# Kernel tuning notes

Hardware: AMD Instinct MI355X
Metric: run time of the kernel (lower is better)

## Reference

```python
import jax, jax.numpy as jnp
import numpy as np

N = 50000        # nodes
DEG = 5          # avg directed degree before symmetrization
F_IN = 512       # node features
HID = 64         # hardcoded hidden width in H2GCN
C = 32           # num_classes
E1_MAX = 800000  # padded 1-hop edge count
E2_MAX = 6000000 # padded 2-hop edge count


def _pad(a, L, dtype):
    out = np.zeros(L, dtype=dtype)
    n = min(len(a), L)
    out[:n] = a[:n]
    return out


def _build_graph(seed=0):
    """Build symmetric 1-hop adjacency A1 (no self loops) and strict 2-hop A2,
    both symmetrically normalized D^-1/2 A D^-1/2, as padded COO edge lists."""
    rng = np.random.default_rng(seed)
    src = rng.integers(0, N, N * DEG)
    dst = rng.integers(0, N, N * DEG)
    row = np.concatenate([src, dst])  # symmetrize
    col = np.concatenate([dst, src])
    m = row != col                    # drop self loops (A - I > 0)
    row, col = row[m], col[m]
    key = np.unique(row.astype(np.int64) * N + col)  # dedupe, sorted by row
    row = (key // N).astype(np.int64)
    col = (key % N).astype(np.int64)
    deg = np.bincount(row, minlength=N)  # symmetric -> row sums == col sums
    dinv = np.where(deg > 0, deg.astype(np.float64) ** -0.5, 0.0).astype(np.float32)
    val1 = dinv[row] * dinv[col]
    # --- compose A@A via CSR expansion (edges sorted by row) ---
    rowptr = np.concatenate([[0], np.cumsum(deg)])
    lens = deg[col]                     # out-degree of each edge's endpoint
    total = int(lens.sum())
    starts = rowptr[col]
    grp = np.repeat(np.cumsum(lens) - lens, lens)
    idx = np.repeat(starts, lens) + (np.arange(total) - grp)
    u2 = np.repeat(row, lens)
    w2 = col[idx]
    key2 = np.unique(u2.astype(np.int64) * N + w2)
    r2 = key2 // N
    c2 = key2 % N
    # strict 2-hop: remove self loops and 1-hop edges
    keep = (r2 != c2) & (~np.isin(key2, key, assume_unique=True))
    r2, c2 = r2[keep], c2[keep]
    deg2 = np.bincount(r2, minlength=N)
    d2inv = np.where(deg2 > 0, deg2.astype(np.float64) ** -0.5, 0.0).astype(np.float32)
    val2 = d2inv[r2] * d2inv[c2]
    return (
        _pad(row, E1_MAX, np.int32), _pad(col, E1_MAX, np.int32), _pad(val1, E1_MAX, np.float32),
        _pad(r2, E2_MAX, np.int32), _pad(c2, E2_MAX, np.int32), _pad(val2, E2_MAX, np.float32),
    )


def setup_inputs() -> dict:
    key = jax.random.key(0)
    k = jax.random.split(key, 6)
    e1r, e1c, e1v, e2r, e2c, e2v = _build_graph(0)
    return {
        "x": jax.random.normal(k[0], (N, F_IN), dtype=jnp.float32),
        "e1_row": jnp.asarray(e1r), "e1_col": jnp.asarray(e1c), "e1_val": jnp.asarray(e1v),
        "e2_row": jnp.asarray(e2r), "e2_col": jnp.asarray(e2c), "e2_val": jnp.asarray(e2v),
        "W1": jax.random.normal(k[1], (F_IN, HID), dtype=jnp.float32) * (1.0 / np.sqrt(F_IN)),
        "b1": jax.random.normal(k[2], (HID,), dtype=jnp.float32) * 0.01,
        "W2": jax.random.normal(k[3], (3 * HID, C), dtype=jnp.float32) * (1.0 / np.sqrt(3 * HID)),
        "b2": jax.random.normal(k[4], (C,), dtype=jnp.float32) * 0.01,
    }


def _spmm(row, col, val, R):
    # sparse [N,N] @ dense [N,H]: gather source rows, scale, scatter-add to dest
    return jax.ops.segment_sum(val[:, None] * R[col], row, num_segments=N)


def reference(x, e1_row, e1_col, e1_val, e2_row, e2_col, e2_val, W1, b1, W2, b2):
    R = jax.nn.relu(x @ W1 + b1)            # [N, 64]
    Rs = [R]
    for _ in range(2):                       # two rounds of hop aggregation
        R1 = _spmm(e1_row, e1_col, e1_val, R)
        R2 = _spmm(e2_row, e2_col, e2_val, R)
        R = jnp.maximum(R1, R2)              # max-pool combine
        Rs.append(R)
    R_final = jnp.concatenate(Rs, axis=1)    # [N, 192]
    # dropout is identity in eval mode
    return jax.nn.log_softmax(R_final @ W2 + b2, axis=1)
```

## Files before the change

### kernel.cpp

```cpp
#include <hip/hip_runtime.h>

#define NN 50000
#define FIN 512
#define HID 64
#define NC 32

__device__ __forceinline__ unsigned short bf16rne(float f) {
  unsigned u = __float_as_uint(f);
  u = u + 0x7FFFu + ((u >> 16) & 1u);
  return (unsigned short)(u >> 16);
}
__device__ __forceinline__ float bf2f(unsigned short s) {
  return __uint_as_float(((unsigned)s) << 16);
}

__global__ __launch_bounds__(256) void gemm1_relu_kernel(
    const float* __restrict__ x, const float* __restrict__ W1,
    const float* __restrict__ b1, float* __restrict__ R0,
    unsigned short* __restrict__ R0b) {
  __shared__ float xs[32][132];
  __shared__ float wsm[32][64];
  const int t = threadIdx.x;
  const int row0 = blockIdx.x * 128;
  const int tr = t >> 4, tc = t & 15;
  float acc[8][4] = {};
  for (int k0 = 0; k0 < FIN; k0 += 32) {
#pragma unroll
    for (int j = 0; j < 4; ++j) {
      const int idx = t + j * 256;
      const int r = idx & 127, kq = idx >> 7;
      float4 xv = make_float4(0.f, 0.f, 0.f, 0.f);
      const int grow = row0 + r;
      if (grow < NN) xv = *(const float4*)(x + (size_t)grow * FIN + k0 + kq * 4);
      xs[kq * 4 + 0][r] = xv.x; xs[kq * 4 + 1][r] = xv.y;
      xs[kq * 4 + 2][r] = xv.z; xs[kq * 4 + 3][r] = xv.w;
    }
#pragma unroll
    for (int j = 0; j < 2; ++j) {
      const int idx = t + j * 256;
      const int wr = idx >> 4, wc = (idx & 15) * 4;
      *(float4*)(&wsm[wr][wc]) = *(const float4*)(W1 + (size_t)(k0 + wr) * HID + wc);
    }
    __syncthreads();
#pragma unroll
    for (int kk = 0; kk < 32; ++kk) {
      const float4 a0 = *(const float4*)(&xs[kk][tr * 8]);
      const float4 a1 = *(const float4*)(&xs[kk][tr * 8 + 4]);
      const float4 b  = *(const float4*)(&wsm[kk][tc * 4]);
      const float av[8] = {a0.x, a0.y, a0.z, a0.w, a1.x, a1.y, a1.z, a1.w};
      const float bv[4] = {b.x, b.y, b.z, b.w};
#pragma unroll
      for (int i = 0; i < 8; ++i)
#pragma unroll
        for (int j = 0; j < 4; ++j) acc[i][j] = fmaf(av[i], bv[j], acc[i][j]);
    }
    __syncthreads();
  }
  const float4 bb = *(const float4*)(b1 + tc * 4);
#pragma unroll
  for (int i = 0; i < 8; ++i) {
    const int grow = row0 + tr * 8 + i;
    if (grow < NN) {
      float4 o;
      o.x = fmaxf(acc[i][0] + bb.x, 0.f);
      o.y = fmaxf(acc[i][1] + bb.y, 0.f);
      o.z = fmaxf(acc[i][2] + bb.z, 0.f);
      o.w = fmaxf(acc[i][3] + bb.w, 0.f);
      *(float4*)(R0 + (size_t)grow * HID + tc * 4) = o;
      uint2 p;
      p.x = ((unsigned)bf16rne(o.y) << 16) | (unsigned)bf16rne(o.x);
      p.y = ((unsigned)bf16rne(o.w) << 16) | (unsigned)bf16rne(o.z);
      *(uint2*)(R0b + (size_t)grow * HID + tc * 4) = p;
    }
  }
}

__global__ void build_rowptr_kernel(const int* __restrict__ row,
                                    const float* __restrict__ val,
                                    const int E, int* __restrict__ ptr) {
  const int e = blockIdx.x * blockDim.x + threadIdx.x;
  if (e >= E) return;
  const int c = (val[e] != 0.f) ? row[e] : NN;
  const int p = (e == 0) ? -1 : ((val[e - 1] != 0.f) ? row[e - 1] : NN);
  for (int r = p + 1; r <= c; ++r) ptr[r] = e;
  if (e == E - 1) {
    for (int r = c + 1; r <= NN; ++r) ptr[r] = E;
  }
}

template <int BLK>
__device__ __forceinline__ float2 seg_pair(const int* __restrict__ col,
                                           const float* __restrict__ val,
                                           int s, int t,
                                           const unsigned short* __restrict__ Rb,
                                           uint2* __restrict__ meta,
                                           const int lane, const unsigned laneoff) {
  float a0 = 0.f, a1 = 0.f;
  const int half = lane >> 5;
  for (int e = s; e < t; e += BLK) {
    const int idx = e + lane;
    if (lane < BLK) {
      unsigned cw = 0u, vw = 0u;
      if (idx < t) { cw = (unsigned)col[idx]; vw = __float_as_uint(val[idx]); }
      meta[lane] = make_uint2(cw, vw);
    }
#pragma unroll
    for (int i = 0; i < BLK / 2; ++i) {
      const uint2 m = meta[2 * i + half];
      const float v = __uint_as_float(m.y);
      const unsigned gw =
          *(const unsigned*)((const char*)Rb + ((size_t)m.x * 128u) + laneoff);
      a0 = fmaf(v, __uint_as_float(gw << 16), a0);
      a1 = fmaf(v, __uint_as_float(gw & 0xffff0000u), a1);
    }
  }
  return make_float2(a0, a1);
}

template <int OUTMODE>
__global__ __launch_bounds__(256) void agg_kernel(
    const int* __restrict__ c1, const float* __restrict__ v1, const int* __restrict__ p1,
    const int* __restrict__ c2, const float* __restrict__ v2, const int* __restrict__ p2,
    const unsigned short* __restrict__ Rb,
    float* __restrict__ outf, unsigned short* __restrict__ outb) {
  __shared__ uint2 meta[4][64];
  const int wslot = threadIdx.x >> 6;
  const int wid = (int)((blockIdx.x * blockDim.x + threadIdx.x) >> 6);
  if (wid >= NN) return;
  const int lane = threadIdx.x & 63;
  const unsigned laneoff = (unsigned)(lane & 31) << 2;
  const float2 h1 = seg_pair<16>(c1, v1, p1[wid], p1[wid + 1], Rb, meta[wslot], lane, laneoff);
  const float2 h2 = seg_pair<64>(c2, v2, p2[wid], p2[wid + 1], Rb, meta[wslot], lane, laneoff);
  const float t1e = h1.x + __shfl_xor(h1.x, 32, 64);
  const float t1o = h1.y + __shfl_xor(h1.y, 32, 64);
  const float t2e = h2.x + __shfl_xor(h2.x, 32, 64);
  const float t2o = h2.y + __shfl_xor(h2.y, 32, 64);
  const int half = lane >> 5;
  const float r = half ? fmaxf(t1o, t2o) : fmaxf(t1e, t2e);
  const size_t oidx = (size_t)wid * HID + 2 * (lane & 31) + half;
  if (OUTMODE == 0) outb[oidx] = bf16rne(r);
  else              outf[oidx] = r;
}

__global__ void final_kernel(const float* __restrict__ R0,
                             const unsigned short* __restrict__ R1b,
                             const float* __restrict__ R2,
                             const float* __restrict__ W2,
                             const float* __restrict__ b2, float* __restrict__ out) {
  __shared__ float w2s[192 * 32];
  __shared__ float fs[8][192];
  const int t = threadIdx.x;
  const int node0 = blockIdx.x * 8;
  for (int i = t; i < 192 * 32; i += 256) w2s[i] = W2[i];
  for (int i = t; i < 8 * 192; i += 256) {
    const int n = i / 192, k = i % 192;
    const int node = node0 + n;
    float v = 0.f;
    if (node < NN) {
      v = (k < 64)  ? R0[(size_t)node * 64 + k]
        : (k < 128) ? bf2f(R1b[(size_t)node * 64 + (k - 64)])
                    : R2[(size_t)node * 64 + (k - 128)];
    }
    fs[n][k] = v;
  }
  __syncthreads();
  const int n = t >> 5, c = t & 31;
  const int node = node0 + n;
  float acc = b2[c];
#pragma unroll 8
  for (int k = 0; k < 192; ++k) acc += fs[n][k] * w2s[k * 32 + c];
  float m = acc;
  for (int off = 16; off; off >>= 1) m = fmaxf(m, __shfl_xor(m, off, 32));
  const float ex = __expf(acc - m);
  float ssum = ex;
  for (int off = 16; off; off >>= 1) ssum += __shfl_xor(ssum, off, 32);
  if (node < NN) out[(size_t)node * 32 + c] = (acc - m) - __logf(ssum);
}

extern "C" void kernel_launch(void* const* d_in, const int* in_sizes, int n_in,
                              void* d_out, int out_size, void* d_ws, size_t ws_size,
                              hipStream_t stream) {
  const float* x  = (const float*)d_in[0];
  const int*   e1r = (const int*)d_in[1];
  const int*   e1c = (const int*)d_in[2];
  const float* e1v = (const float*)d_in[3];
  const int*   e2r = (const int*)d_in[4];
  const int*   e2c = (const int*)d_in[5];
  const float* e2v = (const float*)d_in[6];
  const float* W1 = (const float*)d_in[7];
  const float* b1 = (const float*)d_in[8];
  const float* W2 = (const float*)d_in[9];
  const float* b2 = (const float*)d_in[10];
  float* out = (float*)d_out;
  const int E1 = in_sizes[1];
  const int E2 = in_sizes[4];

  char* wsb = (char*)d_ws;
  const size_t RSZ = (size_t)NN * HID;
  const size_t need = RSZ * 4 * 2 + RSZ * 2 * 2 + 2 * (NN + 1) * sizeof(int);
  if (ws_size < need) return;
  float*          R0  = (float*)wsb;
  float*          R2  = (float*)(wsb + RSZ * 4);
  unsigned short* R0b = (unsigned short*)(wsb + RSZ * 8);
  unsigned short* R1b = (unsigned short*)(wsb + RSZ * 8 + RSZ * 2);
  int*            p1  = (int*)(wsb + RSZ * 8 + RSZ * 4);
  int*            p2  = p1 + (NN + 1);

  gemm1_relu_kernel<<<(NN + 127) / 128, 256, 0, stream>>>(x, W1, b1, R0, R0b);

  build_rowptr_kernel<<<(E1 + 255) / 256, 256, 0, stream>>>(e1r, e1v, E1, p1);
  build_rowptr_kernel<<<(E2 + 255) / 256, 256, 0, stream>>>(e2r, e2v, E2, p2);

  const int aggb = (NN * 64) / 256;
  agg_kernel<0><<<aggb, 256, 0, stream>>>(e1c, e1v, p1, e2c, e2v, p2, R0b, R0, R1b);
  agg_kernel<1><<<aggb, 256, 0, stream>>>(e1c, e1v, p1, e2c, e2v, p2, R1b, R2, R1b);

  final_kernel<<<(NN + 7) / 8, 256, 0, stream>>>(R0, R1b, R2, W2, b2, out);
}
```

Measured before the change: 431.5 us.

## Use bf16 MFMA for the input projection GEMM with prepacked W1

Replaces the fp32 LDS-tiled FMA GEMM for x@W1 with a wave-level MFMA 16x16x32 bf16 kernel. x is converted to bf16 in registers, and W1 is prepacked into the MFMA B-fragment layout by a small new kernel. This aims to cut the compute and shared-memory cost of the first layer so it approaches the bandwidth of reading x. In exchange, inputs are rounded to bf16, and the prepacked buffer sits at an offset that is only 8-byte aligned.

```diff
diff --git a/kernel.cpp b/kernel.cpp
--- a/kernel.cpp
+++ b/kernel.cpp
@@ -5,6 +5,9 @@
 #define HID 64
 #define NC 32
 
+typedef __attribute__((ext_vector_type(8))) short short8;
+typedef __attribute__((ext_vector_type(4))) float f32x4;
+
 __device__ __forceinline__ unsigned short bf16rne(float f) {
   unsigned u = __float_as_uint(f);
   u = u + 0x7FFFu + ((u >> 16) & 1u);
@@ -13,66 +16,76 @@
 __device__ __forceinline__ float bf2f(unsigned short s) {
   return __uint_as_float(((unsigned)s) << 16);
 }
+__device__ __forceinline__ unsigned cvt_pk_bf16(float lo, float hi) {
+  unsigned d;
+  asm("v_cvt_pk_bf16_f32 %0, %1, %2" : "=v"(d) : "v"(lo), "v"(hi));
+  return d;
+}
+
+__global__ void w1_pack_kernel(const float* __restrict__ W1,
+                               unsigned short* __restrict__ W1p) {
+  const int t = blockIdx.x * blockDim.x + threadIdx.x;
+  if (t >= 16 * 4 * 64) return;
+  const int lane = t & 63, nb = (t >> 6) & 3, ks = t >> 8;
+  const int col = nb * 16 + (lane & 15);
+  const int k0 = ks * 32 + (lane >> 4) * 8;
+  float f[8];
+#pragma unroll
+  for (int j = 0; j < 8; ++j) f[j] = W1[(size_t)(k0 + j) * HID + col];
+  uint4 d;
+  d.x = cvt_pk_bf16(f[0], f[1]);
+  d.y = cvt_pk_bf16(f[2], f[3]);
+  d.z = cvt_pk_bf16(f[4], f[5]);
+  d.w = cvt_pk_bf16(f[6], f[7]);
+  *(uint4*)(W1p + (size_t)t * 8) = d;
+}
 
 __global__ __launch_bounds__(256) void gemm1_relu_kernel(
-    const float* __restrict__ x, const float* __restrict__ W1,
+    const float* __restrict__ x, const unsigned short* __restrict__ W1p,
     const float* __restrict__ b1, float* __restrict__ R0,
     unsigned short* __restrict__ R0b) {
-  __shared__ float xs[32][132];
-  __shared__ float wsm[32][64];
   const int t = threadIdx.x;
-  const int row0 = blockIdx.x * 128;
-  const int tr = t >> 4, tc = t & 15;
-  float acc[8][4] = {};
-  for (int k0 = 0; k0 < FIN; k0 += 32) {
+  const int w = t >> 6, lane = t & 63;
+  const int arow = blockIdx.x * 64 + w * 16 + (lane & 15);
+  const size_t rowoff = (arow < NN) ? (size_t)arow * FIN : 0;
+  const float* xp = x + rowoff + (lane >> 4) * 8;
+  f32x4 acc0 = {0.f, 0.f, 0.f, 0.f}, acc1 = acc0, acc2 = acc0, acc3 = acc0;
 #pragma unroll
-    for (int j = 0; j < 4; ++j) {
-      const int idx = t + j * 256;
-      const int r = idx & 127, kq = idx >> 7;
-      float4 xv = make_float4(0.f, 0.f, 0.f, 0.f);
-      const int grow = row0 + r;
-      if (grow < NN) xv = *(const float4*)(x + (size_t)grow * FIN + k0 + kq * 4);
-      xs[kq * 4 + 0][r] = xv.x; xs[kq * 4 + 1][r] = xv.y;
-      xs[kq * 4 + 2][r] = xv.z; xs[kq * 4 + 3][r] = xv.w;
-    }
-#pragma unroll
-    for (int j = 0; j < 2; ++j) {
-      const int idx = t + j * 256;
-      const int wr = idx >> 4, wc = (idx & 15) * 4;
-      *(float4*)(&wsm[wr][wc]) = *(const float4*)(W1 + (size_t)(k0 + wr) * HID + wc);
-    }
-    __syncthreads();
-#pragma unroll
-    for (int kk = 0; kk < 32; ++kk) {
-      const float4 a0 = *(const float4*)(&xs[kk][tr * 8]);
-      const float4 a1 = *(const float4*)(&xs[kk][tr * 8 + 4]);
-      const float4 b  = *(const float4*)(&wsm[kk][tc * 4]);
-      const float av[8] = {a0.x, a0.y, a0.z, a0.w, a1.x, a1.y, a1.z, a1.w};
-      const float bv[4] = {b.x, b.y, b.z, b.w};
-#pragma unroll
-      for (int i = 0; i < 8; ++i)
-#pragma unroll
-        for (int j = 0; j < 4; ++j) acc[i][j] = fmaf(av[i], bv[j], acc[i][j]);
-    }
-    __syncthreads();
-  }
-  const float4 bb = *(const float4*)(b1 + tc * 4);
-#pragma unroll
-  for (int i = 0; i < 8; ++i) {
-    const int grow = row0 + tr * 8 + i;
-    if (grow < NN) {
-      float4 o;
-      o.x = fmaxf(acc[i][0] + bb.x, 0.f);
-      o.y = fmaxf(acc[i][1] + bb.y, 0.f);
-      o.z = fmaxf(acc[i][2] + bb.z, 0.f);
-      o.w = fmaxf(acc[i][3] + bb.w, 0.f);
-      *(float4*)(R0 + (size_t)grow * HID + tc * 4) = o;
-      uint2 p;
-      p.x = ((unsigned)bf16rne(o.y) << 16) | (unsigned)bf16rne(o.x);
-      p.y = ((unsigned)bf16rne(o.w) << 16) | (unsigned)bf16rne(o.z);
-      *(uint2*)(R0b + (size_t)grow * HID + tc * 4) = p;
-    }
-  }
+  for (int ks = 0; ks < 16; ++ks) {
+    const float4 xa = *(const float4*)(xp);
+    const float4 xb = *(const float4*)(xp + 4);
+    xp += 32;
+    uint4 ad;
+    ad.x = cvt_pk_bf16(xa.x, xa.y);
+    ad.y = cvt_pk_bf16(xa.z, xa.w);
+    ad.z = cvt_pk_bf16(xb.x, xb.y);
+    ad.w = cvt_pk_bf16(xb.z, xb.w);
+    const short8 af = __builtin_bit_cast(short8, ad);
+    const short8 b0 = *(const short8*)(W1p + ((size_t)(ks * 4 + 0) * 64 + lane) * 8);
+    const short8 b1f = *(const short8*)(W1p + ((size_t)(ks * 4 + 1) * 64 + lane) * 8);
+    const short8 b2 = *(const short8*)(W1p + ((size_t)(ks * 4 + 2) * 64 + lane) * 8);
+    const short8 b3 = *(const short8*)(W1p + ((size_t)(ks * 4 + 3) * 64 + lane) * 8);
+    acc0 = __builtin_amdgcn_mfma_f32_16x16x32_bf16(af, b0, acc0, 0, 0, 0);
+    acc1 = __builtin_amdgcn_mfma_f32_16x16x32_bf16(af, b1f, acc1, 0, 0, 0);
+    acc2 = __builtin_amdgcn_mfma_f32_16x16x32_bf16(af, b2, acc2, 0, 0, 0);
+    acc3 = __builtin_amdgcn_mfma_f32_16x16x32_bf16(af, b3, acc3, 0, 0, 0);
+  }
+  const int orow = blockIdx.x * 64 + w * 16 + (lane >> 4) * 4;
+  const int ocol = lane & 15;
+#define EPI(NB, ACC)                                                        \
+  {                                                                         \
+    const float bias = b1[NB * 16 + ocol];                                  \
+    _Pragma("unroll") for (int i = 0; i < 4; ++i) {                         \
+      const int r = orow + i;                                               \
+      if (r < NN) {                                                         \
+        const float v = fmaxf(ACC[i] + bias, 0.f);                          \
+        R0[(size_t)r * HID + NB * 16 + ocol] = v;                           \
+        R0b[(size_t)r * HID + NB * 16 + ocol] = bf16rne(v);                 \
+      }                                                                     \
+    }                                                                       \
+  }
+  EPI(0, acc0) EPI(1, acc1) EPI(2, acc2) EPI(3, acc3)
+#undef EPI
 }
 
 __global__ void build_rowptr_kernel(const int* __restrict__ row,
@@ -197,7 +210,8 @@
 
   char* wsb = (char*)d_ws;
   const size_t RSZ = (size_t)NN * HID;
-  const size_t need = RSZ * 4 * 2 + RSZ * 2 * 2 + 2 * (NN + 1) * sizeof(int);
+  const size_t need = RSZ * 4 * 2 + RSZ * 2 * 2 + 2 * (NN + 1) * sizeof(int)
+                    + (size_t)FIN * HID * 2;
   if (ws_size < need) return;
   float*          R0  = (float*)wsb;
   float*          R2  = (float*)(wsb + RSZ * 4);
@@ -205,8 +219,11 @@
   unsigned short* R1b = (unsigned short*)(wsb + RSZ * 8 + RSZ * 2);
   int*            p1  = (int*)(wsb + RSZ * 8 + RSZ * 4);
   int*            p2  = p1 + (NN + 1);
-
-  gemm1_relu_kernel<<<(NN + 127) / 128, 256, 0, stream>>>(x, W1, b1, R0, R0b);
+  unsigned short* W1p = (unsigned short*)(p2 + (NN + 1));
+
+  w1_pack_kernel<<<16, 256, 0, stream>>>(W1, W1p);
+
+  gemm1_relu_kernel<<<(NN + 63) / 64, 256, 0, stream>>>(x, W1p, b1, R0, R0b);
 
   build_rowptr_kernel<<<(E1 + 255) / 256, 256, 0, stream>>>(e1r, e1v, E1, p1);
   build_rowptr_kernel<<<(E2 + 255) / 256, 256, 0, stream>>>(e2r, e2v, E2, p2);
```

Measured after the change: 398.9 us. -7.6%, faster.
